# Kernel tuning notes

Measured on AMD Instinct MI355X. Metric: run time of the kernel, lower is better.

## Reference

```python
import jax, jax.numpy as jnp
import numpy as np

V_W_MAX = 2.2
H = 16777216


def setup_inputs() -> dict:
    key = jax.random.key(0)
    k0, k1 = jax.random.split(key)
    x0 = jax.random.normal(k0, (4,), dtype=jnp.float32)
    U = jax.random.normal(k1, (H, 2), dtype=jnp.float32)
    dt = jnp.float32(0.05)
    return {"x0": x0, "U": U, "dt": dt}


def reference(x0, U, dt):
    # The torch loop has recurrence only in x,y (a running sum); vx,vy depend
    # solely on U[t], so the whole trajectory is elementwise + cumsum.
    vmax = jnp.float32(V_W_MAX)
    uv = jnp.tanh(U) * vmax                       # [H,2] = (vx, vy)
    pos = x0[:2] + jnp.cumsum(uv * dt, axis=0)    # [H,2] integrated x,y
    theta = jnp.arctan2(uv[:, 1], uv[:, 0] + 1e-9)            # [H]
    v = jnp.clip(jnp.sqrt(uv[:, 0] * uv[:, 0] + uv[:, 1] * uv[:, 1] + 1e-12),
                 0.0, vmax)                                    # [H]
    rest = jnp.concatenate([pos, theta[:, None], v[:, None]], axis=1)  # [H,4]
    return jnp.concatenate([x0[None, :], rest], axis=0)       # [H+1,4]
```

## Files before the change

### kernel.cpp

```cpp
#include <hip/hip_runtime.h>
#include <hip/hip_fp16.h>

#define B1 256
#define IT1 8
#define CH1 (B1 * IT1)
#define B2 1024
#define VMAX 2.2f

typedef float f32x4 __attribute__((ext_vector_type(4)));
typedef unsigned u32x4 __attribute__((ext_vector_type(4)));

struct DSum { double x, y; };

__device__ __forceinline__ float fast_tanh(float x) {
  float e = __expf(2.0f * x);
  return 1.0f - 2.0f / (e + 1.0f);
}

__device__ __forceinline__ float fast_atan2(float y, float x) {
  float ax = fabsf(x), ay = fabsf(y);
  float mn = fminf(ax, ay), mx = fmaxf(ax, ay);
  float a = mn / (mx + 1e-30f);
  float s = a * a;
  float r = ((-0.0464964749f * s + 0.15931422f) * s - 0.327622764f) * s * a + a;
  if (ay > ax) r = 1.57079637f - r;
  if (x < 0.0f) r = 3.14159274f - r;
  return copysignf(r, y);
}

__device__ __forceinline__ unsigned packh2(float x, float y) {
  __half2 h = __floats2half2_rn(x, y);
  return *(unsigned*)&h;
}
__device__ __forceinline__ float2 unpackh2(unsigned u) {
  __half2 h = *(__half2*)&u;
  return __half22float2(h);
}

__global__ __launch_bounds__(B1) void wi_prep(
    const float* __restrict__ U, const float* __restrict__ dtp,
    unsigned* __restrict__ uvh, DSum* __restrict__ bsum, int N)
{
  const int t = threadIdx.x;
  const int lane = t & 63, wid = t >> 6;
  const long base = (long)blockIdx.x * CH1 + (long)t * IT1;
  float sx = 0.f, sy = 0.f;
  if (base + IT1 <= (long)N) {
    const f32x4* p = (const f32x4*)(U + 2 * base);
    unsigned pk[IT1];
    #pragma unroll
    for (int i = 0; i < IT1 / 2; ++i) {
      f32x4 a = p[i];
      unsigned q0 = packh2(fast_tanh(a.x) * VMAX, fast_tanh(a.y) * VMAX);
      unsigned q1 = packh2(fast_tanh(a.z) * VMAX, fast_tanh(a.w) * VMAX);
      pk[2*i] = q0; pk[2*i+1] = q1;
      float2 r0 = unpackh2(q0), r1 = unpackh2(q1);
      sx += r0.x + r1.x; sy += r0.y + r1.y;
    }
    u32x4 v0 = { pk[0], pk[1], pk[2], pk[3] };
    u32x4 v1 = { pk[4], pk[5], pk[6], pk[7] };
    *(u32x4*)(uvh + base) = v0;
    *(u32x4*)(uvh + base + 4) = v1;
  } else {
    for (int i = 0; i < IT1; ++i) {
      long idx = base + i;
      if (idx < N) {
        unsigned q = packh2(fast_tanh(U[2*idx]) * VMAX, fast_tanh(U[2*idx+1]) * VMAX);
        uvh[idx] = q;
        float2 r = unpackh2(q);
        sx += r.x; sy += r.y;
      }
    }
  }
  #pragma unroll
  for (int o = 1; o < 64; o <<= 1) { sx += __shfl_xor(sx, o); sy += __shfl_xor(sy, o); }
  __shared__ double wsx[B1/64], wsy[B1/64];
  if (lane == 0) { wsx[wid] = (double)sx; wsy[wid] = (double)sy; }
  __syncthreads();
  if (t == 0) {
    const double dtd = (double)(*dtp);
    double ax = 0.0, ay = 0.0;
    #pragma unroll
    for (int w = 0; w < B1/64; ++w) { ax += wsx[w]; ay += wsy[w]; }
    bsum[blockIdx.x].x = ax * dtd;
    bsum[blockIdx.x].y = ay * dtd;
  }
}

__global__ __launch_bounds__(B2) void wi_scan_blocks(DSum* bsum, int nblocks)
{
  const int t = threadIdx.x;
  const int lane = t & 63, wid = t >> 6;
  const int per = (nblocks + B2 - 1) / B2;
  const int s = t * per;
  const int e = min(s + per, nblocks);
  double tx = 0.0, ty = 0.0;
  for (int i = s; i < e; ++i) { tx += bsum[i].x; ty += bsum[i].y; }
  double ix = tx, iy = ty;
  #pragma unroll
  for (int o = 1; o < 64; o <<= 1) {
    double ux = __shfl_up(ix, o), uy = __shfl_up(iy, o);
    if (lane >= o) { ix += ux; iy += uy; }
  }
  __shared__ double wx[B2/64], wy[B2/64];
  if (lane == 63) { wx[wid] = ix; wy[wid] = iy; }
  __syncthreads();
  double wbx = 0.0, wby = 0.0;
  #pragma unroll
  for (int w = 0; w < B2/64; ++w) {
    if (w < wid) { wbx += wx[w]; wby += wy[w]; }
  }
  double rx = wbx + ix - tx;
  double ry = wby + iy - ty;
  for (int i = s; i < e; ++i) {
    double vx = bsum[i].x, vy = bsum[i].y;
    bsum[i].x = rx; bsum[i].y = ry;
    rx += vx; ry += vy;
  }
}

__global__ __launch_bounds__(B1) void wi_emit_h(
    const unsigned* __restrict__ uvh, const float* __restrict__ x0,
    const float* __restrict__ dtp, const DSum* __restrict__ boff,
    float* __restrict__ out, int N)
{
  __shared__ f32x4 stage[CH1];
  __shared__ float wsum_x[B1/64], wsum_y[B1/64];

  const int t = threadIdx.x;
  const int lane = t & 63, wid = t >> 6;
  const long base = (long)blockIdx.x * CH1 + (long)t * IT1;
  const float dt = *dtp;

  float vx[IT1], vy[IT1];
  const bool full = (base + IT1 <= (long)N);
  if (full) {
    u32x4 v0 = *(const u32x4*)(uvh + base);
    u32x4 v1 = *(const u32x4*)(uvh + base + 4);
    unsigned pk[IT1] = { v0.x, v0.y, v0.z, v0.w, v1.x, v1.y, v1.z, v1.w };
    #pragma unroll
    for (int i = 0; i < IT1; ++i) {
      float2 r = unpackh2(pk[i]);
      vx[i] = r.x; vy[i] = r.y;
    }
  } else {
    for (int i = 0; i < IT1; ++i) {
      long idx = base + i;
      if (idx < N) { float2 r = unpackh2(uvh[idx]); vx[i] = r.x; vy[i] = r.y; }
      else { vx[i] = 0.f; vy[i] = 0.f; }
    }
  }

  float px[IT1], py[IT1];
  float sx = 0.f, sy = 0.f;
  #pragma unroll
  for (int i = 0; i < IT1; ++i) { sx += vx[i]*dt; px[i] = sx; sy += vy[i]*dt; py[i] = sy; }
  const float totx = sx, toty = sy;

  #pragma unroll
  for (int o = 1; o < 64; o <<= 1) {
    float ux = __shfl_up(sx, o), uy = __shfl_up(sy, o);
    if (lane >= o) { sx += ux; sy += uy; }
  }
  if (lane == 63) { wsum_x[wid] = sx; wsum_y[wid] = sy; }
  __syncthreads();
  float wbx = 0.f, wby = 0.f;
  #pragma unroll
  for (int w = 0; w < B1/64; ++w) {
    if (w < wid) { wbx += wsum_x[w]; wby += wsum_y[w]; }
  }
  const float exb = wbx + sx - totx;
  const float eyb = wby + sy - toty;

  const double ox = boff[blockIdx.x].x + (double)x0[0];
  const double oy = boff[blockIdx.x].y + (double)x0[1];

  #pragma unroll
  for (int i = 0; i < IT1; ++i) {
    float posx = (float)(ox + (double)(exb + px[i]));
    float posy = (float)(oy + (double)(eyb + py[i]));
    float th = fast_atan2(vy[i], vx[i] + 1e-9f);
    float vv = fminf(sqrtf(vx[i]*vx[i] + vy[i]*vy[i] + 1e-12f), VMAX);
    f32x4 r; r.x = posx; r.y = posy; r.z = th; r.w = vv;
    const int k = t * IT1 + i;
    stage[k ^ ((k >> 3) & 7)] = r;
  }
  __syncthreads();

  const long tile0 = (long)blockIdx.x * CH1;
  f32x4* o4 = (f32x4*)out;
  #pragma unroll
  for (int i = 0; i < IT1; ++i) {
    const int k = i * B1 + t;
    const long g = tile0 + k;
    if (g < (long)N) __builtin_nontemporal_store(stage[k ^ ((k >> 3) & 7)], o4 + 1 + g);
  }
  if (blockIdx.x == 0 && t == 0) {
    f32x4 r; r.x = x0[0]; r.y = x0[1]; r.z = x0[2]; r.w = x0[3];
    o4[0] = r;
  }
}

__global__ __launch_bounds__(B1) void wi_partial(
    const float* __restrict__ U, const float* __restrict__ dtp,
    DSum* __restrict__ bsum, int N)
{
  const int t = threadIdx.x;
  const int lane = t & 63, wid = t >> 6;
  const long base = (long)blockIdx.x * CH1 + (long)t * IT1;
  float sx = 0.f, sy = 0.f;
  if (base + IT1 <= (long)N) {
    const f32x4* p = (const f32x4*)(U + 2 * base);
    #pragma unroll
    for (int i = 0; i < IT1 / 2; ++i) {
      f32x4 a = p[i];
      sx += fast_tanh(a.x) + fast_tanh(a.z);
      sy += fast_tanh(a.y) + fast_tanh(a.w);
    }
  } else {
    for (int i = 0; i < IT1; ++i) {
      long idx = base + i;
      if (idx < N) { sx += fast_tanh(U[2*idx]); sy += fast_tanh(U[2*idx+1]); }
    }
  }
  #pragma unroll
  for (int o = 1; o < 64; o <<= 1) { sx += __shfl_xor(sx, o); sy += __shfl_xor(sy, o); }
  __shared__ double wsx[B1/64], wsy[B1/64];
  if (lane == 0) { wsx[wid] = (double)sx; wsy[wid] = (double)sy; }
  __syncthreads();
  if (t == 0) {
    const float sc = VMAX * (*dtp);
    double ax = 0.0, ay = 0.0;
    #pragma unroll
    for (int w = 0; w < B1/64; ++w) { ax += wsx[w]; ay += wsy[w]; }
    bsum[blockIdx.x].x = ax * (double)sc;
    bsum[blockIdx.x].y = ay * (double)sc;
  }
}

__global__ __launch_bounds__(B1) void wi_emit(
    const float* __restrict__ U, const float* __restrict__ x0,
    const float* __restrict__ dtp, const DSum* __restrict__ boff,
    float* __restrict__ out, int N)
{
  __shared__ f32x4 stage[CH1];
  __shared__ float wsum_x[B1/64], wsum_y[B1/64];
  const int t = threadIdx.x;
  const int lane = t & 63, wid = t >> 6;
  const long base = (long)blockIdx.x * CH1 + (long)t * IT1;
  const float dt = *dtp;
  float vx[IT1], vy[IT1];
  const bool full = (base + IT1 <= (long)N);
  if (full) {
    const f32x4* p = (const f32x4*)(U + 2 * base);
    #pragma unroll
    for (int i = 0; i < IT1 / 2; ++i) {
      f32x4 a = p[i];
      vx[2*i]   = fast_tanh(a.x) * VMAX; vy[2*i]   = fast_tanh(a.y) * VMAX;
      vx[2*i+1] = fast_tanh(a.z) * VMAX; vy[2*i+1] = fast_tanh(a.w) * VMAX;
    }
  } else {
    for (int i = 0; i < IT1; ++i) {
      long idx = base + i;
      if (idx < N) { vx[i] = fast_tanh(U[2*idx]) * VMAX; vy[i] = fast_tanh(U[2*idx+1]) * VMAX; }
      else { vx[i] = 0.f; vy[i] = 0.f; }
    }
  }
  float px[IT1], py[IT1];
  float sx = 0.f, sy = 0.f;
  #pragma unroll
  for (int i = 0; i < IT1; ++i) { sx += vx[i]*dt; px[i] = sx; sy += vy[i]*dt; py[i] = sy; }
  const float totx = sx, toty = sy;
  #pragma unroll
  for (int o = 1; o < 64; o <<= 1) {
    float ux = __shfl_up(sx, o), uy = __shfl_up(sy, o);
    if (lane >= o) { sx += ux; sy += uy; }
  }
  if (lane == 63) { wsum_x[wid] = sx; wsum_y[wid] = sy; }
  __syncthreads();
  float wbx = 0.f, wby = 0.f;
  #pragma unroll
  for (int w = 0; w < B1/64; ++w) {
    if (w < wid) { wbx += wsum_x[w]; wby += wsum_y[w]; }
  }
  const float exb = wbx + sx - totx;
  const float eyb = wby + sy - toty;
  const double ox = boff[blockIdx.x].x + (double)x0[0];
  const double oy = boff[blockIdx.x].y + (double)x0[1];
  #pragma unroll
  for (int i = 0; i < IT1; ++i) {
    float posx = (float)(ox + (double)(exb + px[i]));
    float posy = (float)(oy + (double)(eyb + py[i]));
    float th = fast_atan2(vy[i], vx[i] + 1e-9f);
    float vv = fminf(sqrtf(vx[i]*vx[i] + vy[i]*vy[i] + 1e-12f), VMAX);
    f32x4 r; r.x = posx; r.y = posy; r.z = th; r.w = vv;
    const int k = t * IT1 + i;
    stage[k ^ ((k >> 3) & 7)] = r;
  }
  __syncthreads();
  const long tile0 = (long)blockIdx.x * CH1;
  f32x4* o4 = (f32x4*)out;
  #pragma unroll
  for (int i = 0; i < IT1; ++i) {
    const int k = i * B1 + t;
    const long g = tile0 + k;
    if (g < (long)N) __builtin_nontemporal_store(stage[k ^ ((k >> 3) & 7)], o4 + 1 + g);
  }
  if (blockIdx.x == 0 && t == 0) {
    f32x4 r; r.x = x0[0]; r.y = x0[1]; r.z = x0[2]; r.w = x0[3];
    o4[0] = r;
  }
}

extern "C" void kernel_launch(void* const* d_in, const int* in_sizes, int n_in,
                              void* d_out, int out_size, void* d_ws, size_t ws_size,
                              hipStream_t stream) {
  const float* x0 = (const float*)d_in[0];
  const float* U  = (const float*)d_in[1];
  const float* dt = (const float*)d_in[2];
  float* out = (float*)d_out;
  const int N = in_sizes[1] / 2;
  const int nb = (N + CH1 - 1) / CH1;

  const size_t uvh_bytes = ((size_t)N * 4 + 255) & ~(size_t)255;
  const size_t needed = uvh_bytes + (size_t)nb * sizeof(DSum);

  if (ws_size >= needed) {
    unsigned* uvh = (unsigned*)d_ws;
    DSum* bsum = (DSum*)((char*)d_ws + uvh_bytes);
    wi_prep<<<nb, B1, 0, stream>>>(U, dt, uvh, bsum, N);
    wi_scan_blocks<<<1, B2, 0, stream>>>(bsum, nb);
    wi_emit_h<<<nb, B1, 0, stream>>>(uvh, x0, dt, bsum, out, N);
  } else {
    DSum* bsum = (DSum*)d_ws;
    wi_partial<<<nb, B1, 0, stream>>>(U, dt, bsum, N);
    wi_scan_blocks<<<1, B2, 0, stream>>>(bsum, nb);
    wi_emit<<<nb, B1, 0, stream>>>(U, x0, dt, bsum, out, N);
  }
}
```

Before: 114.0 us.

## Fuse prep, scan and emit into one cooperative kernel holding values in registers

Replaces the three-kernel pipeline with one cooperative kernel. Each block computes tanh-scaled velocities for its span and keeps them packed in registers. It then publishes block sums, grid-syncs, and computes its prefix offset from the other blocks' sums before emitting outputs in sections. This removes the round trip of the half-precision intermediate through global memory and two kernel launches. The trade-offs are a grid-wide barrier, heavy register use per thread, and per-call host occupancy and device-property queries.

```diff
diff --git a/kernel.cpp b/kernel.cpp
--- a/kernel.cpp
+++ b/kernel.cpp
@@ -1,6 +1,14 @@
 #include <hip/hip_runtime.h>
 #include <hip/hip_fp16.h>
-
+#include <hip/hip_cooperative_groups.h>
+
+#define NB 1024
+#define BT 256
+#define SECS 8
+#define PPS 8
+#define PPT (SECS * PPS)
+#define SEC_PAIRS (BT * PPS)
+#define SPAN (BT * PPT)
 #define B1 256
 #define IT1 8
 #define CH1 (B1 * IT1)
@@ -8,8 +16,6 @@
 #define VMAX 2.2f
 
 typedef float f32x4 __attribute__((ext_vector_type(4)));
-typedef unsigned u32x4 __attribute__((ext_vector_type(4)));
-
 struct DSum { double x, y; };
 
 __device__ __forceinline__ float fast_tanh(float x) {
@@ -37,9 +43,146 @@
   return __half22float2(h);
 }
 
-__global__ __launch_bounds__(B1) void wi_prep(
+__global__ __launch_bounds__(BT, 4) void wi_fused(
+    const float* __restrict__ U, const float* __restrict__ x0,
+    const float* __restrict__ dtp, DSum* __restrict__ bsum,
+    float* __restrict__ out, int N)
+{
+  namespace cg = cooperative_groups;
+  cg::grid_group grid = cg::this_grid();
+
+  const int b = blockIdx.x;
+  const int t = threadIdx.x;
+  const int lane = t & 63, wid = t >> 6;
+  const long Bb = (long)b * SPAN;
+
+  __shared__ f32x4 stage[SEC_PAIRS];
+  __shared__ double wsx[BT / 64], wsy[BT / 64];
+  __shared__ float swx[BT / 64], swy[BT / 64];
+  __shared__ double s_ox, s_oy, s_dtd;
+
+  unsigned pk[PPT];
+  float tsx = 0.f, tsy = 0.f;
+
+  #pragma unroll
+  for (int s = 0; s < SECS; ++s) {
+    const long g0 = Bb + (long)s * SEC_PAIRS + (long)t * PPS;
+    const f32x4* pbase = (const f32x4*)(U + 2 * g0);
+    #pragma unroll
+    for (int i = 0; i < PPS / 2; ++i) {
+      const long p0 = g0 + 2 * i;
+      f32x4 a;
+      if (p0 + 2 <= (long)N) {
+        a = pbase[i];
+      } else {
+        a.x = (p0 < (long)N)     ? U[2*p0]   : 0.f;
+        a.y = (p0 < (long)N)     ? U[2*p0+1] : 0.f;
+        a.z = (p0 + 1 < (long)N) ? U[2*p0+2] : 0.f;
+        a.w = (p0 + 1 < (long)N) ? U[2*p0+3] : 0.f;
+      }
+      unsigned q0 = packh2(fast_tanh(a.x) * VMAX, fast_tanh(a.y) * VMAX);
+      unsigned q1 = packh2(fast_tanh(a.z) * VMAX, fast_tanh(a.w) * VMAX);
+      pk[s * PPS + 2 * i]     = q0;
+      pk[s * PPS + 2 * i + 1] = q1;
+      float2 r0 = unpackh2(q0), r1 = unpackh2(q1);
+      tsx += r0.x + r1.x; tsy += r0.y + r1.y;
+    }
+  }
+  {
+    float rx = tsx, ry = tsy;
+    #pragma unroll
+    for (int o = 1; o < 64; o <<= 1) { rx += __shfl_xor(rx, o); ry += __shfl_xor(ry, o); }
+    if (lane == 0) { wsx[wid] = (double)rx; wsy[wid] = (double)ry; }
+    __syncthreads();
+    if (t == 0) {
+      double ax = 0.0, ay = 0.0;
+      #pragma unroll
+      for (int w = 0; w < BT / 64; ++w) { ax += wsx[w]; ay += wsy[w]; }
+      bsum[b].x = ax; bsum[b].y = ay;
+    }
+  }
+  __threadfence();
+  grid.sync();
+
+  if (wid == 0) {
+    double px = 0.0, py = 0.0;
+    const int i0 = lane * (NB / 64);
+    #pragma unroll
+    for (int j = 0; j < NB / 64; ++j) {
+      const int i = i0 + j;
+      if (i < b) { px += bsum[i].x; py += bsum[i].y; }
+    }
+    #pragma unroll
+    for (int o = 1; o < 64; o <<= 1) { px += __shfl_xor(px, o); py += __shfl_xor(py, o); }
+    if (lane == 0) {
+      const double dtd = (double)(*dtp);
+      s_ox = (double)x0[0] + px * dtd;
+      s_oy = (double)x0[1] + py * dtd;
+      s_dtd = dtd;
+    }
+  }
+  __syncthreads();
+  const double ox = s_ox, oy = s_oy, dtd = s_dtd;
+
+  f32x4* o4 = (f32x4*)out;
+  if (b == 0 && t == 0) {
+    f32x4 r; r.x = x0[0]; r.y = x0[1]; r.z = x0[2]; r.w = x0[3];
+    o4[0] = r;
+  }
+  float carx = 0.f, cary = 0.f;
+  #pragma unroll
+  for (int s = 0; s < SECS; ++s) {
+    float ssx = 0.f, ssy = 0.f;
+    #pragma unroll
+    for (int k = 0; k < PPS; ++k) {
+      float2 r = unpackh2(pk[s * PPS + k]);
+      ssx += r.x; ssy += r.y;
+    }
+    float isx = ssx, isy = ssy;
+    #pragma unroll
+    for (int o = 1; o < 64; o <<= 1) {
+      float ux = __shfl_up(isx, o), uy = __shfl_up(isy, o);
+      if (lane >= o) { isx += ux; isy += uy; }
+    }
+    if (lane == 63) { swx[wid] = isx; swy[wid] = isy; }
+    __syncthreads();
+    float wox = 0.f, woy = 0.f, stx = 0.f, sty = 0.f;
+    #pragma unroll
+    for (int w = 0; w < BT / 64; ++w) {
+      float a = swx[w], c = swy[w];
+      if (w < wid) { wox += a; woy += c; }
+      stx += a; sty += c;
+    }
+    float offx = carx + wox + (isx - ssx);
+    float offy = cary + woy + (isy - ssy);
+    carx += stx; cary += sty;
+    #pragma unroll
+    for (int k = 0; k < PPS; ++k) {
+      float2 rr = unpackh2(pk[s * PPS + k]);
+      offx += rr.x; offy += rr.y;
+      float posx = (float)(ox + (double)offx * dtd);
+      float posy = (float)(oy + (double)offy * dtd);
+      float th = fast_atan2(rr.y, rr.x + 1e-9f);
+      float vv = fminf(sqrtf(rr.x * rr.x + rr.y * rr.y + 1e-12f), VMAX);
+      f32x4 r; r.x = posx; r.y = posy; r.z = th; r.w = vv;
+      const int kk = t * PPS + k;
+      stage[kk ^ ((kk >> 3) & 7)] = r;
+    }
+    __syncthreads();
+    const long sb = Bb + (long)s * SEC_PAIRS;
+    #pragma unroll
+    for (int i = 0; i < PPS; ++i) {
+      const int kk = i * BT + t;
+      const long g = sb + kk;
+      if (g < (long)N) __builtin_nontemporal_store(stage[kk ^ ((kk >> 3) & 7)], o4 + 1 + g);
+    }
+    __syncthreads();
+  }
+}
+
+__global__ __launch_bounds__(B1) void wi_partial(
     const float* __restrict__ U, const float* __restrict__ dtp,
-    unsigned* __restrict__ uvh, DSum* __restrict__ bsum, int N)
+    DSum* __restrict__ bsum, int N)
 {
   const int t = threadIdx.x;
   const int lane = t & 63, wid = t >> 6;
@@ -47,29 +190,16 @@
   float sx = 0.f, sy = 0.f;
   if (base + IT1 <= (long)N) {
     const f32x4* p = (const f32x4*)(U + 2 * base);
-    unsigned pk[IT1];
     #pragma unroll
     for (int i = 0; i < IT1 / 2; ++i) {
       f32x4 a = p[i];
-      unsigned q0 = packh2(fast_tanh(a.x) * VMAX, fast_tanh(a.y) * VMAX);
-      unsigned q1 = packh2(fast_tanh(a.z) * VMAX, fast_tanh(a.w) * VMAX);
-      pk[2*i] = q0; pk[2*i+1] = q1;
-      float2 r0 = unpackh2(q0), r1 = unpackh2(q1);
-      sx += r0.x + r1.x; sy += r0.y + r1.y;
-    }
-    u32x4 v0 = { pk[0], pk[1], pk[2], pk[3] };
-    u32x4 v1 = { pk[4], pk[5], pk[6], pk[7] };
-    *(u32x4*)(uvh + base) = v0;
-    *(u32x4*)(uvh + base + 4) = v1;
+      sx += fast_tanh(a.x) + fast_tanh(a.z);
+      sy += fast_tanh(a.y) + fast_tanh(a.w);
+    }
   } else {
     for (int i = 0; i < IT1; ++i) {
       long idx = base + i;
-      if (idx < N) {
-        unsigned q = packh2(fast_tanh(U[2*idx]) * VMAX, fast_tanh(U[2*idx+1]) * VMAX);
-        uvh[idx] = q;
-        float2 r = unpackh2(q);
-        sx += r.x; sy += r.y;
-      }
+      if (idx < N) { sx += fast_tanh(U[2*idx]); sy += fast_tanh(U[2*idx+1]); }
     }
   }
   #pragma unroll
@@ -78,12 +208,12 @@
   if (lane == 0) { wsx[wid] = (double)sx; wsy[wid] = (double)sy; }
   __syncthreads();
   if (t == 0) {
-    const double dtd = (double)(*dtp);
+    const float sc = VMAX * (*dtp);
     double ax = 0.0, ay = 0.0;
     #pragma unroll
     for (int w = 0; w < B1/64; ++w) { ax += wsx[w]; ay += wsy[w]; }
-    bsum[blockIdx.x].x = ax * dtd;
-    bsum[blockIdx.x].y = ay * dtd;
+    bsum[blockIdx.x].x = ax * (double)sc;
+    bsum[blockIdx.x].y = ay * (double)sc;
   }
 }
 
@@ -116,125 +246,6 @@
     double vx = bsum[i].x, vy = bsum[i].y;
     bsum[i].x = rx; bsum[i].y = ry;
     rx += vx; ry += vy;
-  }
-}
-
-__global__ __launch_bounds__(B1) void wi_emit_h(
-    const unsigned* __restrict__ uvh, const float* __restrict__ x0,
-    const float* __restrict__ dtp, const DSum* __restrict__ boff,
-    float* __restrict__ out, int N)
-{
-  __shared__ f32x4 stage[CH1];
-  __shared__ float wsum_x[B1/64], wsum_y[B1/64];
-
-  const int t = threadIdx.x;
-  const int lane = t & 63, wid = t >> 6;
-  const long base = (long)blockIdx.x * CH1 + (long)t * IT1;
-  const float dt = *dtp;
-
-  float vx[IT1], vy[IT1];
-  const bool full = (base + IT1 <= (long)N);
-  if (full) {
-    u32x4 v0 = *(const u32x4*)(uvh + base);
-    u32x4 v1 = *(const u32x4*)(uvh + base + 4);
-    unsigned pk[IT1] = { v0.x, v0.y, v0.z, v0.w, v1.x, v1.y, v1.z, v1.w };
-    #pragma unroll
-    for (int i = 0; i < IT1; ++i) {
-      float2 r = unpackh2(pk[i]);
-      vx[i] = r.x; vy[i] = r.y;
-    }
-  } else {
-    for (int i = 0; i < IT1; ++i) {
-      long idx = base + i;
-      if (idx < N) { float2 r = unpackh2(uvh[idx]); vx[i] = r.x; vy[i] = r.y; }
-      else { vx[i] = 0.f; vy[i] = 0.f; }
-    }
-  }
-
-  float px[IT1], py[IT1];
-  float sx = 0.f, sy = 0.f;
-  #pragma unroll
-  for (int i = 0; i < IT1; ++i) { sx += vx[i]*dt; px[i] = sx; sy += vy[i]*dt; py[i] = sy; }
-  const float totx = sx, toty = sy;
-
-  #pragma unroll
-  for (int o = 1; o < 64; o <<= 1) {
-    float ux = __shfl_up(sx, o), uy = __shfl_up(sy, o);
-    if (lane >= o) { sx += ux; sy += uy; }
-  }
-  if (lane == 63) { wsum_x[wid] = sx; wsum_y[wid] = sy; }
-  __syncthreads();
-  float wbx = 0.f, wby = 0.f;
-  #pragma unroll
-  for (int w = 0; w < B1/64; ++w) {
-    if (w < wid) { wbx += wsum_x[w]; wby += wsum_y[w]; }
-  }
-  const float exb = wbx + sx - totx;
-  const float eyb = wby + sy - toty;
-
-  const double ox = boff[blockIdx.x].x + (double)x0[0];
-  const double oy = boff[blockIdx.x].y + (double)x0[1];
-
-  #pragma unroll
-  for (int i = 0; i < IT1; ++i) {
-    float posx = (float)(ox + (double)(exb + px[i]));
-    float posy = (float)(oy + (double)(eyb + py[i]));
-    float th = fast_atan2(vy[i], vx[i] + 1e-9f);
-    float vv = fminf(sqrtf(vx[i]*vx[i] + vy[i]*vy[i] + 1e-12f), VMAX);
-    f32x4 r; r.x = posx; r.y = posy; r.z = th; r.w = vv;
-    const int k = t * IT1 + i;
-    stage[k ^ ((k >> 3) & 7)] = r;
-  }
-  __syncthreads();
-
-  const long tile0 = (long)blockIdx.x * CH1;
-  f32x4* o4 = (f32x4*)out;
-  #pragma unroll
-  for (int i = 0; i < IT1; ++i) {
-    const int k = i * B1 + t;
-    const long g = tile0 + k;
-    if (g < (long)N) __builtin_nontemporal_store(stage[k ^ ((k >> 3) & 7)], o4 + 1 + g);
-  }
-  if (blockIdx.x == 0 && t == 0) {
-    f32x4 r; r.x = x0[0]; r.y = x0[1]; r.z = x0[2]; r.w = x0[3];
-    o4[0] = r;
-  }
-}
-
-__global__ __launch_bounds__(B1) void wi_partial(
-    const float* __restrict__ U, const float* __restrict__ dtp,
-    DSum* __restrict__ bsum, int N)
-{
-  const int t = threadIdx.x;
-  const int lane = t & 63, wid = t >> 6;
-  const long base = (long)blockIdx.x * CH1 + (long)t * IT1;
-  float sx = 0.f, sy = 0.f;
-  if (base + IT1 <= (long)N) {
-    const f32x4* p = (const f32x4*)(U + 2 * base);
-    #pragma unroll
-    for (int i = 0; i < IT1 / 2; ++i) {
-      f32x4 a = p[i];
-      sx += fast_tanh(a.x) + fast_tanh(a.z);
-      sy += fast_tanh(a.y) + fast_tanh(a.w);
-    }
-  } else {
-    for (int i = 0; i < IT1; ++i) {
-      long idx = base + i;
-      if (idx < N) { sx += fast_tanh(U[2*idx]); sy += fast_tanh(U[2*idx+1]); }
-    }
-  }
-  #pragma unroll
-  for (int o = 1; o < 64; o <<= 1) { sx += __shfl_xor(sx, o); sy += __shfl_xor(sy, o); }
-  __shared__ double wsx[B1/64], wsy[B1/64];
-  if (lane == 0) { wsx[wid] = (double)sx; wsy[wid] = (double)sy; }
-  __syncthreads();
-  if (t == 0) {
-    const float sc = VMAX * (*dtp);
-    double ax = 0.0, ay = 0.0;
-    #pragma unroll
-    for (int w = 0; w < B1/64; ++w) { ax += wsx[w]; ay += wsy[w]; }
-    bsum[blockIdx.x].x = ax * (double)sc;
-    bsum[blockIdx.x].y = ay * (double)sc;
   }
 }
 
@@ -320,21 +331,25 @@
   const float* dt = (const float*)d_in[2];
   float* out = (float*)d_out;
   const int N = in_sizes[1] / 2;
+  DSum* bsum = (DSum*)d_ws;
+
+  int maxPerCU = 0;
+  hipError_t qerr = hipOccupancyMaxActiveBlocksPerMultiprocessor(&maxPerCU, wi_fused, BT, 0);
+  int numCU = 0;
+  hipDeviceProp_t props;
+  if (hipGetDeviceProperties(&props, 0) == hipSuccess) numCU = props.multiProcessorCount;
+
+  bool coop_ok = (qerr == hipSuccess) && (N <= NB * SPAN) &&
+                 ((long)maxPerCU * numCU >= NB);
+  if (coop_ok) {
+    void* args[] = { (void*)&U, (void*)&x0, (void*)&dt, (void*)&bsum, (void*)&out, (void*)&N };
+    hipError_t lerr = hipLaunchCooperativeKernel((void*)wi_fused, dim3(NB), dim3(BT),
+                                                 args, 0, stream);
+    if (lerr == hipSuccess) return;
+  }
+
   const int nb = (N + CH1 - 1) / CH1;
-
-  const size_t uvh_bytes = ((size_t)N * 4 + 255) & ~(size_t)255;
-  const size_t needed = uvh_bytes + (size_t)nb * sizeof(DSum);
-
-  if (ws_size >= needed) {
-    unsigned* uvh = (unsigned*)d_ws;
-    DSum* bsum = (DSum*)((char*)d_ws + uvh_bytes);
-    wi_prep<<<nb, B1, 0, stream>>>(U, dt, uvh, bsum, N);
-    wi_scan_blocks<<<1, B2, 0, stream>>>(bsum, nb);
-    wi_emit_h<<<nb, B1, 0, stream>>>(uvh, x0, dt, bsum, out, N);
-  } else {
-    DSum* bsum = (DSum*)d_ws;
-    wi_partial<<<nb, B1, 0, stream>>>(U, dt, bsum, N);
-    wi_scan_blocks<<<1, B2, 0, stream>>>(bsum, nb);
-    wi_emit<<<nb, B1, 0, stream>>>(U, x0, dt, bsum, out, N);
-  }
-}
+  wi_partial<<<nb, B1, 0, stream>>>(U, dt, bsum, N);
+  wi_scan_blocks<<<1, B2, 0, stream>>>(bsum, nb);
+  wi_emit<<<nb, B1, 0, stream>>>(U, x0, dt, bsum, out, N);
+}
```

Result: faster. 108.3 us (-5.0%).
